# Kernel optimization log

Hardware: AMD Instinct MI355X
Metric: run time of the kernel (lower is better)

## Reference

```python
import jax, jax.numpy as jnp
import numpy as np

B, C = 2048, 5000          # batchSize, classNum
LLR_REL = 0.9              # keep-rate; k = ceil(B*C*(1-llr_rel))
K = int(np.ceil(B * C * (1.0 - LLR_REL)))
MARGIN = 0.0


def _bce_with_logits(x, t):
    # elementwise BCEWithLogitsLoss (reduce=False): max(x,0) - x*t + log1p(exp(-|x|))
    return jnp.maximum(x, 0.0) - x * t + jnp.log1p(jnp.exp(-jnp.abs(x)))


def setup_inputs() -> dict:
    key = jax.random.key(0)
    k1, k2 = jax.random.split(key)
    inp = jax.random.normal(k1, (B, C), dtype=jnp.float32)
    # target in {-1, 0, +1}: -1 negative, 0 unobserved/ignored, +1 positive
    tgt = (jax.random.randint(k2, (B, C), 0, 3) - 1).astype(jnp.float32)
    return {"input": inp, "target": tgt, "k": K}


def reference(input, target, k):
    input = input.astype(jnp.float32)
    target = target.astype(jnp.float32)
    positive_mask = (target > MARGIN).astype(jnp.float32)
    negative_mask = (target < -MARGIN).astype(jnp.float32)
    positive_loss = _bce_with_logits(input, target)
    negative_loss = _bce_with_logits(-input, -target)
    unobserved_loss = negative_mask * negative_loss
    if k != 0:
        # k-th largest value of the flattened unobserved loss is the threshold
        topk_vals = jax.lax.top_k(unobserved_loss.reshape(-1), k)[0]
        topk_lossvalue = topk_vals[-1]
        loss_mask = (unobserved_loss < topk_lossvalue).astype(jnp.float32)
        negative_mask = negative_mask * loss_mask
    loss = positive_mask * positive_loss + negative_mask * negative_loss
    return loss
```

## Files before the change

kernel.cpp:

```cpp
#include <hip/hip_runtime.h>
#include <cstdint>


struct SelState {
    uint32_t prefix;
    uint32_t k_rem;
    uint32_t u_kth;
    float    thr_nl;
    uint32_t done;
};

#define GUARD 256u

__device__ __forceinline__ uint32_t xform(uint32_t b) {
    return ((int32_t)b < 0) ? ~b : (b | 0x80000000u);
}
__device__ __forceinline__ float unxform(uint32_t u) {
    uint32_t b = (u & 0x80000000u) ? (u ^ 0x80000000u) : ~u;
    return __uint_as_float(b);
}
__device__ __forceinline__ float neg_loss_precise(float x, float t) {
#pragma clang fp contract(off)
    return (fmaxf(-x, 0.0f) - x * t) + log1pf(expf(-fabsf(x)));
}

__global__ __launch_bounds__(256) void k1_compact(
        const float* __restrict__ x, const float* __restrict__ t,
        uint32_t* __restrict__ comp, uint32_t* __restrict__ bcount,
        uint32_t cap, int n) {
    const int n4 = n >> 2;
    const int S = gridDim.x * 256;
    uint32_t* __restrict__ seg = comp + (size_t)blockIdx.x * cap;
    uint32_t* __restrict__ cur = &bcount[blockIdx.x];
    const float4* __restrict__ x4 = (const float4*)x;
    const float4* __restrict__ t4 = (const float4*)t;
    const int lane = threadIdx.x & 63;

    for (int ib = blockIdx.x * 256; ib < n4; ib += 2 * S) {
        const int i1 = ib + threadIdx.x;
        const int i2 = i1 + S;
        const bool v1 = i1 < n4, v2 = i2 < n4;
        float4 xa, ta, xb, tb;
        if (v1) { xa = x4[i1]; ta = t4[i1]; }
        if (v2) { xb = x4[i2]; tb = t4[i2]; }
        uint32_t loc[8];
        int c = 0;
        if (v1) {
            uint32_t u;
            u = (ta.x < 0.0f) ? xform(__float_as_uint(xa.x)) : 0u; if (u) loc[c++] = u;
            u = (ta.y < 0.0f) ? xform(__float_as_uint(xa.y)) : 0u; if (u) loc[c++] = u;
            u = (ta.z < 0.0f) ? xform(__float_as_uint(xa.z)) : 0u; if (u) loc[c++] = u;
            u = (ta.w < 0.0f) ? xform(__float_as_uint(xa.w)) : 0u; if (u) loc[c++] = u;
        }
        if (v2) {
            uint32_t u;
            u = (tb.x < 0.0f) ? xform(__float_as_uint(xb.x)) : 0u; if (u) loc[c++] = u;
            u = (tb.y < 0.0f) ? xform(__float_as_uint(xb.y)) : 0u; if (u) loc[c++] = u;
            u = (tb.z < 0.0f) ? xform(__float_as_uint(xb.z)) : 0u; if (u) loc[c++] = u;
            u = (tb.w < 0.0f) ? xform(__float_as_uint(xb.w)) : 0u; if (u) loc[c++] = u;
        }
        if (__ballot(c > 0)) {
            int pfx = c;
#pragma unroll
            for (int off = 1; off < 64; off <<= 1) {
                int vv = __shfl_up(pfx, off);
                if (lane >= off) pfx += vv;
            }
            const int tot = __shfl(pfx, 63);
            uint32_t base = 0;
            if (lane == 63) base = atomicAdd(cur, (uint32_t)tot);
            base = __shfl(base, 63);
            uint32_t o = base + (uint32_t)(pfx - c);
            for (int j = 0; j < c; ++j) seg[o + j] = loc[j];
        }
    }
    if (blockIdx.x == 0) {
        const int j = (n4 << 2) + threadIdx.x;
        uint32_t u = 0;
        if (j < n && t[j] < 0.0f) u = xform(__float_as_uint(x[j]));
        const int c = u ? 1 : 0;
        if (__ballot(c > 0)) {
            int pfx = c;
#pragma unroll
            for (int off = 1; off < 64; off <<= 1) {
                int vv = __shfl_up(pfx, off);
                if (lane >= off) pfx += vv;
            }
            const int tot = __shfl(pfx, 63);
            uint32_t base = 0;
            if (lane == 63) base = atomicAdd(cur, (uint32_t)tot);
            base = __shfl(base, 63);
            if (c) seg[base + (uint32_t)(pfx - 1)] = u;
        }
    }
}

__global__ __launch_bounds__(256) void k1b_hist(
        const uint32_t* __restrict__ comp, const uint32_t* __restrict__ bcount,
        uint32_t cap, uint32_t* __restrict__ hist,
        const float* __restrict__ x, const float* __restrict__ t, int n) {
    __shared__ uint32_t lh[2 * 2048];
    for (int i = threadIdx.x; i < 2 * 2048; i += 256) lh[i] = 0;
    __syncthreads();
    uint32_t* my = &lh[(threadIdx.x & 1) * 2048];

    if (comp) {
        const uint32_t cnt = bcount[blockIdx.x];
        const uint32_t* __restrict__ seg = comp + (size_t)blockIdx.x * cap;
        uint32_t j = threadIdx.x;
        for (; j + 768u < cnt; j += 1024u) {
            uint32_t a = seg[j], b = seg[j + 256], c = seg[j + 512], d = seg[j + 768];
            atomicAdd(&my[a >> 21], 1u);
            atomicAdd(&my[b >> 21], 1u);
            atomicAdd(&my[c >> 21], 1u);
            atomicAdd(&my[d >> 21], 1u);
        }
        for (; j < cnt; j += 256u) atomicAdd(&my[seg[j] >> 21], 1u);
    } else {
        const float4* x4 = (const float4*)x;
        const float4* t4 = (const float4*)t;
        const int n4 = n >> 2;
        const int S = gridDim.x * 256;
        for (int i = blockIdx.x * 256 + threadIdx.x; i < n4; i += S) {
            float4 xv = x4[i], tv = t4[i];
            uint32_t u;
            u = (tv.x < 0.0f) ? xform(__float_as_uint(xv.x)) : 0u; if (u) atomicAdd(&my[u >> 21], 1u);
            u = (tv.y < 0.0f) ? xform(__float_as_uint(xv.y)) : 0u; if (u) atomicAdd(&my[u >> 21], 1u);
            u = (tv.z < 0.0f) ? xform(__float_as_uint(xv.z)) : 0u; if (u) atomicAdd(&my[u >> 21], 1u);
            u = (tv.w < 0.0f) ? xform(__float_as_uint(xv.w)) : 0u; if (u) atomicAdd(&my[u >> 21], 1u);
        }
        if (blockIdx.x == 0) {
            for (int j = (n4 << 2) + threadIdx.x; j < n; j += 256) {
                uint32_t u = (t[j] < 0.0f) ? xform(__float_as_uint(x[j])) : 0u;
                if (u) atomicAdd(&my[u >> 21], 1u);
            }
        }
    }
    __syncthreads();
    for (int b = threadIdx.x; b < 2048; b += 256) {
        uint32_t c = lh[b] + lh[2048 + b];
        if (c) atomicAdd(&hist[b], c);
    }
}

__global__ __launch_bounds__(256) void scan1(
        const uint32_t* __restrict__ hist, SelState* __restrict__ st,
        const int* __restrict__ kptr) {
    __shared__ uint32_t part[256];
    const int tid = threadIdx.x;
    uint32_t cnt[8];
    uint32_t lsum = 0;
#pragma unroll
    for (int j = 0; j < 8; ++j) { cnt[j] = hist[tid * 8 + j]; lsum += cnt[j]; }
    part[tid] = lsum;
    __syncthreads();
    for (int off = 1; off < 256; off <<= 1) {
        uint32_t add = (tid + off < 256) ? part[tid + off] : 0u;
        __syncthreads();
        part[tid] += add;
        __syncthreads();
    }
    const uint32_t total = part[0];
    int kk = *kptr;
    uint32_t k = (kk > 0) ? (uint32_t)kk : 0u;
    if (k == 0u) {
        if (tid == 0) { st->u_kth = 0xFFFFFFFFu; st->thr_nl = __int_as_float(0x7F800000); st->done = 1u; }
        return;
    }
    if (k > total) {
        if (tid == 0) { st->u_kth = 0u; st->thr_nl = 0.0f; st->done = 1u; }
        return;
    }
    uint32_t A = (tid < 255) ? part[tid + 1] : 0u;
#pragma unroll
    for (int j = 7; j >= 0; --j) {
        uint32_t c = cnt[j];
        if (A < k && k <= A + c) {
            st->prefix = (uint32_t)(tid * 8 + j);
            st->k_rem = k - A;
        }
        A += c;
    }
}

__global__ __launch_bounds__(256) void k2_hist21(
        const uint32_t* __restrict__ comp, const uint32_t* __restrict__ bcount,
        uint32_t cap, uint32_t* __restrict__ h21, const SelState* __restrict__ st,
        const float* __restrict__ x, const float* __restrict__ t, int n) {
    __shared__ uint32_t s_pref, s_done;
    if (threadIdx.x == 0) { s_pref = st->prefix; s_done = st->done; }
    __syncthreads();
    if (s_done) return;
    const uint32_t pref = s_pref;

    if (comp) {
        const uint32_t cnt = bcount[blockIdx.x];
        const uint32_t* __restrict__ seg = comp + (size_t)blockIdx.x * cap;
        uint32_t j = threadIdx.x;
        for (; j + 768u < cnt; j += 1024u) {
            uint32_t a = seg[j], b = seg[j + 256], c = seg[j + 512], d = seg[j + 768];
            if ((a >> 21) == pref) atomicAdd(&h21[a & 0x1FFFFFu], 1u);
            if ((b >> 21) == pref) atomicAdd(&h21[b & 0x1FFFFFu], 1u);
            if ((c >> 21) == pref) atomicAdd(&h21[c & 0x1FFFFFu], 1u);
            if ((d >> 21) == pref) atomicAdd(&h21[d & 0x1FFFFFu], 1u);
        }
        for (; j < cnt; j += 256u) {
            uint32_t a = seg[j];
            if ((a >> 21) == pref) atomicAdd(&h21[a & 0x1FFFFFu], 1u);
        }
    } else {
        const float4* x4 = (const float4*)x;
        const float4* t4 = (const float4*)t;
        const int n4 = n >> 2;
        const int S = gridDim.x * 256;
        for (int i = blockIdx.x * 256 + threadIdx.x; i < n4; i += S) {
            float4 xv = x4[i], tv = t4[i];
            uint32_t u;
            u = (tv.x < 0.0f) ? xform(__float_as_uint(xv.x)) : 0u;
            if (u && (u >> 21) == pref) atomicAdd(&h21[u & 0x1FFFFFu], 1u);
            u = (tv.y < 0.0f) ? xform(__float_as_uint(xv.y)) : 0u;
            if (u && (u >> 21) == pref) atomicAdd(&h21[u & 0x1FFFFFu], 1u);
            u = (tv.z < 0.0f) ? xform(__float_as_uint(xv.z)) : 0u;
            if (u && (u >> 21) == pref) atomicAdd(&h21[u & 0x1FFFFFu], 1u);
            u = (tv.w < 0.0f) ? xform(__float_as_uint(xv.w)) : 0u;
            if (u && (u >> 21) == pref) atomicAdd(&h21[u & 0x1FFFFFu], 1u);
        }
        if (blockIdx.x == 0) {
            for (int j = (n4 << 2) + threadIdx.x; j < n; j += 256) {
                uint32_t u = (t[j] < 0.0f) ? xform(__float_as_uint(x[j])) : 0u;
                if (u && (u >> 21) == pref) atomicAdd(&h21[u & 0x1FFFFFu], 1u);
            }
        }
    }
}

__global__ __launch_bounds__(256) void scan2a(
        const uint32_t* __restrict__ h21, uint32_t* __restrict__ csums,
        const SelState* __restrict__ st) {
    __shared__ uint32_t red[256];
    __shared__ uint32_t s_done;
    if (threadIdx.x == 0) s_done = st->done;
    __syncthreads();
    if (s_done) return;
    const uint4* b4 = (const uint4*)(h21 + (size_t)blockIdx.x * 2048);
    uint32_t s = 0;
    for (int j = threadIdx.x; j < 512; j += 256) {
        uint4 v = b4[j];
        s += v.x + v.y + v.z + v.w;
    }
    red[threadIdx.x] = s;
    __syncthreads();
    for (int off = 128; off > 0; off >>= 1) {
        if (threadIdx.x < off) red[threadIdx.x] += red[threadIdx.x + off];
        __syncthreads();
    }
    if (threadIdx.x == 0) csums[blockIdx.x] = red[0];
}

__global__ __launch_bounds__(256) void scan2b(
        const uint32_t* __restrict__ h21, const uint32_t* __restrict__ csums,
        SelState* __restrict__ st) {
    __shared__ uint32_t part[256];
    __shared__ uint32_t sel[2];
    __shared__ SelState sst;
    const int tid = threadIdx.x;
    if (tid == 0) sst = *st;
    __syncthreads();
    if (sst.done) return;
    const uint32_t k = sst.k_rem;

    uint32_t c4[4];
    uint32_t lsum = 0;
#pragma unroll
    for (int j = 0; j < 4; ++j) { c4[j] = csums[tid * 4 + j]; lsum += c4[j]; }
    part[tid] = lsum;
    __syncthreads();
    for (int off = 1; off < 256; off <<= 1) {
        uint32_t add = (tid + off < 256) ? part[tid + off] : 0u;
        __syncthreads();
        part[tid] += add;
        __syncthreads();
    }
    uint32_t A = (tid < 255) ? part[tid + 1] : 0u;
#pragma unroll
    for (int j = 3; j >= 0; --j) {
        uint32_t c = c4[j];
        if (A < k && k <= A + c) { sel[0] = (uint32_t)(tid * 4 + j); sel[1] = k - A; }
        A += c;
    }
    __syncthreads();
    const uint32_t chunk = sel[0];
    const uint32_t k2 = sel[1];
    __syncthreads();

    const uint32_t* base = h21 + (size_t)chunk * 2048;
    uint32_t b8[8];
    lsum = 0;
#pragma unroll
    for (int j = 0; j < 8; ++j) { b8[j] = base[tid * 8 + j]; lsum += b8[j]; }
    part[tid] = lsum;
    __syncthreads();
    for (int off = 1; off < 256; off <<= 1) {
        uint32_t add = (tid + off < 256) ? part[tid + off] : 0u;
        __syncthreads();
        part[tid] += add;
        __syncthreads();
    }
    A = (tid < 255) ? part[tid + 1] : 0u;
#pragma unroll
    for (int j = 7; j >= 0; --j) {
        uint32_t c = b8[j];
        if (A < k2 && k2 <= A + c) {
            uint32_t u = (sst.prefix << 21) | (chunk * 2048u + (uint32_t)(tid * 8 + j));
            st->u_kth = u;
            st->thr_nl = neg_loss_precise(unxform(u), -1.0f);
            st->done = 1u;
        }
        A += c;
    }
}

__device__ __forceinline__ float fin1(float xx, float tt, uint32_t ukth, float thr) {
    float lp = __logf(1.0f + __expf(-fabsf(xx)));
    float v = 0.0f;
    if (tt > 0.0f) {
        v = fmaxf(xx, 0.0f) - xx * tt + lp;
    } else if (tt < 0.0f) {
        uint32_t u = xform(__float_as_uint(xx));
        bool keep = u < ukth;
        if (keep && (ukth - u) < GUARD)
            keep = neg_loss_precise(xx, tt) < thr;
        if (keep) v = fmaxf(-xx, 0.0f) - xx * tt + lp;
    }
    return v;
}

__device__ __forceinline__ float4 fin_quad(float4 xv, float4 tv, uint32_t ukth, float thr) {
    float4 r;
    r.x = fin1(xv.x, tv.x, ukth, thr);
    r.y = fin1(xv.y, tv.y, ukth, thr);
    r.z = fin1(xv.z, tv.z, ukth, thr);
    r.w = fin1(xv.w, tv.w, ukth, thr);
    return r;
}

__global__ __launch_bounds__(256) void k_final(
        const float* __restrict__ x, const float* __restrict__ t,
        const SelState* __restrict__ st, float* __restrict__ out, int n) {
    const uint32_t ukth = st->u_kth;
    const float thr = st->thr_nl;
    const float4* x4 = (const float4*)x;
    const float4* t4 = (const float4*)t;
    float4* o4 = (float4*)out;
    const int n4 = n >> 2;
    const int S = gridDim.x * 256;
    int i = blockIdx.x * 256 + threadIdx.x;
    for (; i + 3 * S < n4; i += 4 * S) {
        float4 xa = x4[i], xb = x4[i + S], xc = x4[i + 2 * S], xd = x4[i + 3 * S];
        float4 ta = t4[i], tb = t4[i + S], tc = t4[i + 2 * S], td = t4[i + 3 * S];
        o4[i]         = fin_quad(xa, ta, ukth, thr);
        o4[i + S]     = fin_quad(xb, tb, ukth, thr);
        o4[i + 2 * S] = fin_quad(xc, tc, ukth, thr);
        o4[i + 3 * S] = fin_quad(xd, td, ukth, thr);
    }
    for (; i < n4; i += S) {
        float4 xa = x4[i], ta = t4[i];
        o4[i] = fin_quad(xa, ta, ukth, thr);
    }
    if (blockIdx.x == 0) {
        for (int j = (n4 << 2) + threadIdx.x; j < n; j += 256) {
            out[j] = fin1(x[j], t[j], ukth, thr);
        }
    }
}

extern "C" void kernel_launch(void* const* d_in, const int* in_sizes, int n_in,
                              void* d_out, int out_size, void* d_ws, size_t ws_size,
                              hipStream_t stream) {
    const float* x = (const float*)d_in[0];
    const float* t = (const float*)d_in[1];
    const int* kptr = (const int*)d_in[2];
    float* out = (float*)d_out;
    const int n = in_sizes[0];
    if (n <= 0) return;

    char* ws = (char*)d_ws;
    uint32_t* hist1 = (uint32_t*)(ws + 0);
    uint32_t* csums = (uint32_t*)(ws + 8192);
    SelState* st    = (SelState*)(ws + 12288);
    uint32_t* bcnt  = (uint32_t*)(ws + 16384);
    uint32_t* h21   = (uint32_t*)(ws + 32768);
    const size_t h21_end = 32768 + (size_t)(1u << 21) * 4u;

    const int n4 = n >> 2;
    int work = (n4 + 255) / 256;
    if (work < 1) work = 1;
    const int grid1 = work < 2048 ? work : 2048;
    const int gridF = work < 2048 ? work : 2048;

    const int S = grid1 * 256;
    const uint32_t iters = (uint32_t)((n4 + 2 * S - 1) / (2 * S));
    uint32_t cap = iters * 8u * 256u + 8u;
    const size_t need = h21_end + (size_t)cap * 4u * (size_t)grid1;
    uint32_t* comp = (ws_size >= need) ? (uint32_t*)(ws + h21_end) : nullptr;

    hipMemsetAsync(d_ws, 0, h21_end, stream);

    if (comp)
        k1_compact<<<grid1, 256, 0, stream>>>(x, t, comp, bcnt, cap, n);
    k1b_hist <<<grid1, 256, 0, stream>>>(comp, bcnt, cap, hist1, x, t, n);
    scan1    <<<1, 256, 0, stream>>>(hist1, st, kptr);
    k2_hist21<<<grid1, 256, 0, stream>>>(comp, bcnt, cap, h21, st, x, t, n);
    scan2a   <<<1024, 256, 0, stream>>>(h21, csums, st);
    scan2b   <<<1, 256, 0, stream>>>(h21, csums, st);
    k_final  <<<gridF, 256, 0, stream>>>(x, t, st, out, n);
}
```

Before: 194.9 us.

## Build 21-bit radix histogram during compaction and recompute selection in consumer kernels

The radix select is restructured. The compaction kernel now builds the high-21-bit histogram directly with global atomics, replacing the 11-bit first pass. The second pass only histograms the low 11 bits of the matching bucket. The separate scan kernels and the SelState struct are removed: each block of k2_low and k_final redundantly runs the prefix-scan selection prologue, cutting the chain from seven launches to four. The cost is about 5M scattered global atomics into a 2M-entry histogram, plus a repeated three-stage scan in every block of the final kernel.

```diff
diff --git a/kernel.cpp b/kernel.cpp
--- a/kernel.cpp
+++ b/kernel.cpp
@@ -1,14 +1,6 @@
 #include <hip/hip_runtime.h>
 #include <cstdint>
 
-
-struct SelState {
-    uint32_t prefix;
-    uint32_t k_rem;
-    uint32_t u_kth;
-    float    thr_nl;
-    uint32_t done;
-};
 
 #define GUARD 256u
 
@@ -19,18 +11,18 @@
     uint32_t b = (u & 0x80000000u) ? (u ^ 0x80000000u) : ~u;
     return __uint_as_float(b);
 }
-__device__ __forceinline__ float neg_loss_precise(float x, float t) {
+__device__ __forceinline__ float neg_loss_precise(float xx, float tt) {
 #pragma clang fp contract(off)
-    return (fmaxf(-x, 0.0f) - x * t) + log1pf(expf(-fabsf(x)));
+    return (fmaxf(-xx, 0.0f) - xx * tt) + log1pf(expf(-fabsf(xx)));
 }
 
 __global__ __launch_bounds__(256) void k1_compact(
         const float* __restrict__ x, const float* __restrict__ t,
         uint32_t* __restrict__ comp, uint32_t* __restrict__ bcount,
-        uint32_t cap, int n) {
+        uint32_t* __restrict__ h21, uint32_t cap, int n) {
     const int n4 = n >> 2;
     const int S = gridDim.x * 256;
-    uint32_t* __restrict__ seg = comp + (size_t)blockIdx.x * cap;
+    uint32_t* __restrict__ seg = comp ? comp + (size_t)blockIdx.x * cap : nullptr;
     uint32_t* __restrict__ cur = &bcount[blockIdx.x];
     const float4* __restrict__ x4 = (const float4*)x;
     const float4* __restrict__ t4 = (const float4*)t;
@@ -59,7 +51,8 @@
             u = (tb.z < 0.0f) ? xform(__float_as_uint(xb.z)) : 0u; if (u) loc[c++] = u;
             u = (tb.w < 0.0f) ? xform(__float_as_uint(xb.w)) : 0u; if (u) loc[c++] = u;
         }
-        if (__ballot(c > 0)) {
+        for (int j = 0; j < c; ++j) atomicAdd(&h21[loc[j] >> 11], 1u);
+        if (seg && __ballot(c > 0)) {
             int pfx = c;
 #pragma unroll
             for (int off = 1; off < 64; off <<= 1) {
@@ -78,8 +71,9 @@
         const int j = (n4 << 2) + threadIdx.x;
         uint32_t u = 0;
         if (j < n && t[j] < 0.0f) u = xform(__float_as_uint(x[j]));
+        if (u) atomicAdd(&h21[u >> 11], 1u);
         const int c = u ? 1 : 0;
-        if (__ballot(c > 0)) {
+        if (seg && __ballot(c > 0)) {
             int pfx = c;
 #pragma unroll
             for (int off = 1; off < 64; off <<= 1) {
@@ -95,14 +89,89 @@
     }
 }
 
-__global__ __launch_bounds__(256) void k1b_hist(
+__global__ __launch_bounds__(256) void scanA(
+        const uint32_t* __restrict__ h21, uint32_t* __restrict__ csums) {
+    __shared__ uint32_t red[256];
+    const uint4* b4 = (const uint4*)(h21 + (size_t)blockIdx.x * 2048);
+    uint32_t s = 0;
+    for (int j = threadIdx.x; j < 512; j += 256) {
+        uint4 v = b4[j];
+        s += v.x + v.y + v.z + v.w;
+    }
+    red[threadIdx.x] = s;
+    __syncthreads();
+    for (int off = 128; off > 0; off >>= 1) {
+        if (threadIdx.x < off) red[threadIdx.x] += red[threadIdx.x + off];
+        __syncthreads();
+    }
+    if (threadIdx.x == 0) csums[blockIdx.x] = red[0];
+}
+
+template<int CH>
+__device__ void pick_kth(const uint32_t* __restrict__ h, uint32_t k,
+                         uint32_t* part, uint32_t* sel) {
+    const int tid = threadIdx.x;
+    uint32_t cnt[CH];
+    uint32_t lsum = 0;
+#pragma unroll
+    for (int j = 0; j < CH; ++j) { cnt[j] = h[tid * CH + j]; lsum += cnt[j]; }
+    part[tid] = lsum;
+    __syncthreads();
+    for (int off = 1; off < 256; off <<= 1) {
+        uint32_t add = (tid + off < 256) ? part[tid + off] : 0u;
+        __syncthreads();
+        part[tid] += add;
+        __syncthreads();
+    }
+    if (tid == 0) sel[2] = part[0];
+    uint32_t A = (tid < 255) ? part[tid + 1] : 0u;
+#pragma unroll
+    for (int j = CH - 1; j >= 0; --j) {
+        uint32_t c = cnt[j];
+        if (A < k && k <= A + c) { sel[0] = (uint32_t)(tid * CH + j); sel[1] = k - A; }
+        A += c;
+    }
+    __syncthreads();
+}
+
+__device__ int sel_prologue(const uint32_t* __restrict__ h21,
+                            const uint32_t* __restrict__ csums,
+                            const uint32_t* __restrict__ hist2,
+                            const int* __restrict__ kptr, int mode,
+                            uint32_t* part, uint32_t* sel,
+                            uint32_t* p21_out, uint32_t* ukth, float* thr) {
+    int kk = *kptr;
+    if (kk <= 0) { *ukth = 0xFFFFFFFFu; *thr = __int_as_float(0x7F800000); return 1; }
+    const uint32_t k = (uint32_t)kk;
+    pick_kth<4>(csums, k, part, sel);
+    if (k > sel[2]) { *ukth = 0u; *thr = 0.0f; return 2; }
+    const uint32_t chunk = sel[0];
+    const uint32_t kA = sel[1];
+    __syncthreads();
+    pick_kth<8>(h21 + (size_t)chunk * 2048u, kA, part, sel);
+    const uint32_t p21 = chunk * 2048u + sel[0];
+    const uint32_t kB = sel[1];
+    *p21_out = p21;
+    if (mode == 1) return 0;
+    __syncthreads();
+    pick_kth<8>(hist2, kB, part, sel);
+    const uint32_t u = (p21 << 11) | sel[0];
+    *ukth = u;
+    *thr = neg_loss_precise(unxform(u), -1.0f);
+    return 0;
+}
+
+__global__ __launch_bounds__(256) void k2_low(
         const uint32_t* __restrict__ comp, const uint32_t* __restrict__ bcount,
-        uint32_t cap, uint32_t* __restrict__ hist,
+        uint32_t cap, const uint32_t* __restrict__ h21,
+        const uint32_t* __restrict__ csums, uint32_t* __restrict__ hist2,
+        const int* __restrict__ kptr,
         const float* __restrict__ x, const float* __restrict__ t, int n) {
-    __shared__ uint32_t lh[2 * 2048];
-    for (int i = threadIdx.x; i < 2 * 2048; i += 256) lh[i] = 0;
-    __syncthreads();
-    uint32_t* my = &lh[(threadIdx.x & 1) * 2048];
+    __shared__ uint32_t part[256];
+    __shared__ uint32_t sel[3];
+    uint32_t p21 = 0, ukth; float thr;
+    if (sel_prologue(h21, csums, nullptr, kptr, 1, part, sel, &p21, &ukth, &thr))
+        return;
 
     if (comp) {
         const uint32_t cnt = bcount[blockIdx.x];
@@ -110,103 +179,14 @@
         uint32_t j = threadIdx.x;
         for (; j + 768u < cnt; j += 1024u) {
             uint32_t a = seg[j], b = seg[j + 256], c = seg[j + 512], d = seg[j + 768];
-            atomicAdd(&my[a >> 21], 1u);
-            atomicAdd(&my[b >> 21], 1u);
-            atomicAdd(&my[c >> 21], 1u);
-            atomicAdd(&my[d >> 21], 1u);
-        }
-        for (; j < cnt; j += 256u) atomicAdd(&my[seg[j] >> 21], 1u);
-    } else {
-        const float4* x4 = (const float4*)x;
-        const float4* t4 = (const float4*)t;
-        const int n4 = n >> 2;
-        const int S = gridDim.x * 256;
-        for (int i = blockIdx.x * 256 + threadIdx.x; i < n4; i += S) {
-            float4 xv = x4[i], tv = t4[i];
-            uint32_t u;
-            u = (tv.x < 0.0f) ? xform(__float_as_uint(xv.x)) : 0u; if (u) atomicAdd(&my[u >> 21], 1u);
-            u = (tv.y < 0.0f) ? xform(__float_as_uint(xv.y)) : 0u; if (u) atomicAdd(&my[u >> 21], 1u);
-            u = (tv.z < 0.0f) ? xform(__float_as_uint(xv.z)) : 0u; if (u) atomicAdd(&my[u >> 21], 1u);
-            u = (tv.w < 0.0f) ? xform(__float_as_uint(xv.w)) : 0u; if (u) atomicAdd(&my[u >> 21], 1u);
-        }
-        if (blockIdx.x == 0) {
-            for (int j = (n4 << 2) + threadIdx.x; j < n; j += 256) {
-                uint32_t u = (t[j] < 0.0f) ? xform(__float_as_uint(x[j])) : 0u;
-                if (u) atomicAdd(&my[u >> 21], 1u);
-            }
-        }
-    }
-    __syncthreads();
-    for (int b = threadIdx.x; b < 2048; b += 256) {
-        uint32_t c = lh[b] + lh[2048 + b];
-        if (c) atomicAdd(&hist[b], c);
-    }
-}
-
-__global__ __launch_bounds__(256) void scan1(
-        const uint32_t* __restrict__ hist, SelState* __restrict__ st,
-        const int* __restrict__ kptr) {
-    __shared__ uint32_t part[256];
-    const int tid = threadIdx.x;
-    uint32_t cnt[8];
-    uint32_t lsum = 0;
-#pragma unroll
-    for (int j = 0; j < 8; ++j) { cnt[j] = hist[tid * 8 + j]; lsum += cnt[j]; }
-    part[tid] = lsum;
-    __syncthreads();
-    for (int off = 1; off < 256; off <<= 1) {
-        uint32_t add = (tid + off < 256) ? part[tid + off] : 0u;
-        __syncthreads();
-        part[tid] += add;
-        __syncthreads();
-    }
-    const uint32_t total = part[0];
-    int kk = *kptr;
-    uint32_t k = (kk > 0) ? (uint32_t)kk : 0u;
-    if (k == 0u) {
-        if (tid == 0) { st->u_kth = 0xFFFFFFFFu; st->thr_nl = __int_as_float(0x7F800000); st->done = 1u; }
-        return;
-    }
-    if (k > total) {
-        if (tid == 0) { st->u_kth = 0u; st->thr_nl = 0.0f; st->done = 1u; }
-        return;
-    }
-    uint32_t A = (tid < 255) ? part[tid + 1] : 0u;
-#pragma unroll
-    for (int j = 7; j >= 0; --j) {
-        uint32_t c = cnt[j];
-        if (A < k && k <= A + c) {
-            st->prefix = (uint32_t)(tid * 8 + j);
-            st->k_rem = k - A;
-        }
-        A += c;
-    }
-}
-
-__global__ __launch_bounds__(256) void k2_hist21(
-        const uint32_t* __restrict__ comp, const uint32_t* __restrict__ bcount,
-        uint32_t cap, uint32_t* __restrict__ h21, const SelState* __restrict__ st,
-        const float* __restrict__ x, const float* __restrict__ t, int n) {
-    __shared__ uint32_t s_pref, s_done;
-    if (threadIdx.x == 0) { s_pref = st->prefix; s_done = st->done; }
-    __syncthreads();
-    if (s_done) return;
-    const uint32_t pref = s_pref;
-
-    if (comp) {
-        const uint32_t cnt = bcount[blockIdx.x];
-        const uint32_t* __restrict__ seg = comp + (size_t)blockIdx.x * cap;
-        uint32_t j = threadIdx.x;
-        for (; j + 768u < cnt; j += 1024u) {
-            uint32_t a = seg[j], b = seg[j + 256], c = seg[j + 512], d = seg[j + 768];
-            if ((a >> 21) == pref) atomicAdd(&h21[a & 0x1FFFFFu], 1u);
-            if ((b >> 21) == pref) atomicAdd(&h21[b & 0x1FFFFFu], 1u);
-            if ((c >> 21) == pref) atomicAdd(&h21[c & 0x1FFFFFu], 1u);
-            if ((d >> 21) == pref) atomicAdd(&h21[d & 0x1FFFFFu], 1u);
+            if ((a >> 11) == p21) atomicAdd(&hist2[a & 0x7FFu], 1u);
+            if ((b >> 11) == p21) atomicAdd(&hist2[b & 0x7FFu], 1u);
+            if ((c >> 11) == p21) atomicAdd(&hist2[c & 0x7FFu], 1u);
+            if ((d >> 11) == p21) atomicAdd(&hist2[d & 0x7FFu], 1u);
         }
         for (; j < cnt; j += 256u) {
             uint32_t a = seg[j];
-            if ((a >> 21) == pref) atomicAdd(&h21[a & 0x1FFFFFu], 1u);
+            if ((a >> 11) == p21) atomicAdd(&hist2[a & 0x7FFu], 1u);
         }
     } else {
         const float4* x4 = (const float4*)x;
@@ -217,106 +197,20 @@
             float4 xv = x4[i], tv = t4[i];
             uint32_t u;
             u = (tv.x < 0.0f) ? xform(__float_as_uint(xv.x)) : 0u;
-            if (u && (u >> 21) == pref) atomicAdd(&h21[u & 0x1FFFFFu], 1u);
+            if (u && (u >> 11) == p21) atomicAdd(&hist2[u & 0x7FFu], 1u);
             u = (tv.y < 0.0f) ? xform(__float_as_uint(xv.y)) : 0u;
-            if (u && (u >> 21) == pref) atomicAdd(&h21[u & 0x1FFFFFu], 1u);
+            if (u && (u >> 11) == p21) atomicAdd(&hist2[u & 0x7FFu], 1u);
             u = (tv.z < 0.0f) ? xform(__float_as_uint(xv.z)) : 0u;
-            if (u && (u >> 21) == pref) atomicAdd(&h21[u & 0x1FFFFFu], 1u);
+            if (u && (u >> 11) == p21) atomicAdd(&hist2[u & 0x7FFu], 1u);
             u = (tv.w < 0.0f) ? xform(__float_as_uint(xv.w)) : 0u;
-            if (u && (u >> 21) == pref) atomicAdd(&h21[u & 0x1FFFFFu], 1u);
+            if (u && (u >> 11) == p21) atomicAdd(&hist2[u & 0x7FFu], 1u);
         }
         if (blockIdx.x == 0) {
             for (int j = (n4 << 2) + threadIdx.x; j < n; j += 256) {
                 uint32_t u = (t[j] < 0.0f) ? xform(__float_as_uint(x[j])) : 0u;
-                if (u && (u >> 21) == pref) atomicAdd(&h21[u & 0x1FFFFFu], 1u);
+                if (u && (u >> 11) == p21) atomicAdd(&hist2[u & 0x7FFu], 1u);
             }
         }
-    }
-}
-
-__global__ __launch_bounds__(256) void scan2a(
-        const uint32_t* __restrict__ h21, uint32_t* __restrict__ csums,
-        const SelState* __restrict__ st) {
-    __shared__ uint32_t red[256];
-    __shared__ uint32_t s_done;
-    if (threadIdx.x == 0) s_done = st->done;
-    __syncthreads();
-    if (s_done) return;
-    const uint4* b4 = (const uint4*)(h21 + (size_t)blockIdx.x * 2048);
-    uint32_t s = 0;
-    for (int j = threadIdx.x; j < 512; j += 256) {
-        uint4 v = b4[j];
-        s += v.x + v.y + v.z + v.w;
-    }
-    red[threadIdx.x] = s;
-    __syncthreads();
-    for (int off = 128; off > 0; off >>= 1) {
-        if (threadIdx.x < off) red[threadIdx.x] += red[threadIdx.x + off];
-        __syncthreads();
-    }
-    if (threadIdx.x == 0) csums[blockIdx.x] = red[0];
-}
-
-__global__ __launch_bounds__(256) void scan2b(
-        const uint32_t* __restrict__ h21, const uint32_t* __restrict__ csums,
-        SelState* __restrict__ st) {
-    __shared__ uint32_t part[256];
-    __shared__ uint32_t sel[2];
-    __shared__ SelState sst;
-    const int tid = threadIdx.x;
-    if (tid == 0) sst = *st;
-    __syncthreads();
-    if (sst.done) return;
-    const uint32_t k = sst.k_rem;
-
-    uint32_t c4[4];
-    uint32_t lsum = 0;
-#pragma unroll
-    for (int j = 0; j < 4; ++j) { c4[j] = csums[tid * 4 + j]; lsum += c4[j]; }
-    part[tid] = lsum;
-    __syncthreads();
-    for (int off = 1; off < 256; off <<= 1) {
-        uint32_t add = (tid + off < 256) ? part[tid + off] : 0u;
-        __syncthreads();
-        part[tid] += add;
-        __syncthreads();
-    }
-    uint32_t A = (tid < 255) ? part[tid + 1] : 0u;
-#pragma unroll
-    for (int j = 3; j >= 0; --j) {
-        uint32_t c = c4[j];
-        if (A < k && k <= A + c) { sel[0] = (uint32_t)(tid * 4 + j); sel[1] = k - A; }
-        A += c;
-    }
-    __syncthreads();
-    const uint32_t chunk = sel[0];
-    const uint32_t k2 = sel[1];
-    __syncthreads();
-
-    const uint32_t* base = h21 + (size_t)chunk * 2048;
-    uint32_t b8[8];
-    lsum = 0;
-#pragma unroll
-    for (int j = 0; j < 8; ++j) { b8[j] = base[tid * 8 + j]; lsum += b8[j]; }
-    part[tid] = lsum;
-    __syncthreads();
-    for (int off = 1; off < 256; off <<= 1) {
-        uint32_t add = (tid + off < 256) ? part[tid + off] : 0u;
-        __syncthreads();
-        part[tid] += add;
-        __syncthreads();
-    }
-    A = (tid < 255) ? part[tid + 1] : 0u;
-#pragma unroll
-    for (int j = 7; j >= 0; --j) {
-        uint32_t c = b8[j];
-        if (A < k2 && k2 <= A + c) {
-            uint32_t u = (sst.prefix << 21) | (chunk * 2048u + (uint32_t)(tid * 8 + j));
-            st->u_kth = u;
-            st->thr_nl = neg_loss_precise(unxform(u), -1.0f);
-            st->done = 1u;
-        }
-        A += c;
     }
 }
 
@@ -346,9 +240,14 @@
 
 __global__ __launch_bounds__(256) void k_final(
         const float* __restrict__ x, const float* __restrict__ t,
-        const SelState* __restrict__ st, float* __restrict__ out, int n) {
-    const uint32_t ukth = st->u_kth;
-    const float thr = st->thr_nl;
+        const uint32_t* __restrict__ h21, const uint32_t* __restrict__ csums,
+        const uint32_t* __restrict__ hist2, const int* __restrict__ kptr,
+        float* __restrict__ out, int n) {
+    __shared__ uint32_t part[256];
+    __shared__ uint32_t sel[3];
+    uint32_t p21, ukth = 0; float thr = 0.0f;
+    sel_prologue(h21, csums, hist2, kptr, 2, part, sel, &p21, &ukth, &thr);
+
     const float4* x4 = (const float4*)x;
     const float4* t4 = (const float4*)t;
     float4* o4 = (float4*)out;
@@ -385,10 +284,9 @@
     if (n <= 0) return;
 
     char* ws = (char*)d_ws;
-    uint32_t* hist1 = (uint32_t*)(ws + 0);
-    uint32_t* csums = (uint32_t*)(ws + 8192);
-    SelState* st    = (SelState*)(ws + 12288);
-    uint32_t* bcnt  = (uint32_t*)(ws + 16384);
+    uint32_t* csums = (uint32_t*)(ws + 0);
+    uint32_t* hist2 = (uint32_t*)(ws + 4096);
+    uint32_t* bcnt  = (uint32_t*)(ws + 12288);
     uint32_t* h21   = (uint32_t*)(ws + 32768);
     const size_t h21_end = 32768 + (size_t)(1u << 21) * 4u;
 
@@ -400,18 +298,14 @@
 
     const int S = grid1 * 256;
     const uint32_t iters = (uint32_t)((n4 + 2 * S - 1) / (2 * S));
-    uint32_t cap = iters * 8u * 256u + 8u;
+    const uint32_t cap = iters * 2048u + 8u;
     const size_t need = h21_end + (size_t)cap * 4u * (size_t)grid1;
     uint32_t* comp = (ws_size >= need) ? (uint32_t*)(ws + h21_end) : nullptr;
 
     hipMemsetAsync(d_ws, 0, h21_end, stream);
 
-    if (comp)
-        k1_compact<<<grid1, 256, 0, stream>>>(x, t, comp, bcnt, cap, n);
-    k1b_hist <<<grid1, 256, 0, stream>>>(comp, bcnt, cap, hist1, x, t, n);
-    scan1    <<<1, 256, 0, stream>>>(hist1, st, kptr);
-    k2_hist21<<<grid1, 256, 0, stream>>>(comp, bcnt, cap, h21, st, x, t, n);
-    scan2a   <<<1024, 256, 0, stream>>>(h21, csums, st);
-    scan2b   <<<1, 256, 0, stream>>>(h21, csums, st);
-    k_final  <<<gridF, 256, 0, stream>>>(x, t, st, out, n);
-}
+    k1_compact<<<grid1, 256, 0, stream>>>(x, t, comp, bcnt, h21, cap, n);
+    scanA     <<<1024, 256, 0, stream>>>(h21, csums);
+    k2_low    <<<grid1, 256, 0, stream>>>(comp, bcnt, cap, h21, csums, hist2, kptr, x, t, n);
+    k_final   <<<gridF, 256, 0, stream>>>(x, t, h21, csums, hist2, kptr, out, n);
+}
```

Result: slower. 298.7 us (+53.3%).
